# Optimization experiments

Hardware: AMD Instinct MI355X
Metric: run time of the kernel (lower is better)

The kernel has to match this reference:

```python
import jax, jax.numpy as jnp
import numpy as np

N = 8192
F_IN = 512
F_OUT = 512
DENSITY = 0.01


def setup_inputs() -> dict:
    key = jax.random.key(0)
    k_x, k_adj, k_w, k_b = jax.random.split(key, 4)
    input_features = jax.random.normal(k_x, (N, F_IN), dtype=jnp.float32)
    adj = (jax.random.uniform(k_adj, (N, N)) < DENSITY).astype(jnp.float32)
    idx = jnp.arange(N)
    adj = adj.at[idx, idx].set(1.0)
    # nn.Linear(in, out) params; W stored as [in, out] so hidden = x @ W + b
    W = jax.random.normal(k_w, (F_IN, F_OUT), dtype=jnp.float32) / np.sqrt(F_IN)
    b = jax.random.normal(k_b, (F_OUT,), dtype=jnp.float32) * 0.01
    return {"input_features": input_features, "adj": adj, "W": W, "b": b}


def reference(input_features, adj, W, b):
    # adj.to_dense().bool().float(): binarize any nonzero entry
    A = (adj != 0).astype(input_features.dtype)  # [N, N]
    hidden = input_features @ W + b              # [N, F_out]
    deg = jnp.sum(A, axis=0)                     # column sums, [N]
    return (A @ hidden) / deg[:, None]           # [N, F_out]
```

## Files before the change

### kernel.cpp

```cpp
#include <hip/hip_runtime.h>
#include <stdint.h>

#define N_NODES 8192
#define FEAT 512

__device__ __forceinline__ unsigned short f2bf(float f) {
  unsigned int u = __float_as_uint(f);
  u += 0x7fffu + ((u >> 16) & 1u);
  return (unsigned short)(u >> 16);
}
__device__ __forceinline__ float bflo(unsigned int u) { return __uint_as_float(u << 16); }
__device__ __forceinline__ float bfhi(unsigned int u) { return __uint_as_float(u & 0xffff0000u); }

typedef __attribute__((ext_vector_type(8))) short short8;
typedef __attribute__((ext_vector_type(4))) float floatx4;

__global__ __launch_bounds__(256) void prep_kernel(const float* __restrict__ W,
                                                   unsigned short* __restrict__ Wt,
                                                   unsigned int* __restrict__ deg) {
  int gid = blockIdx.x * 256 + threadIdx.x;
  int k = gid >> 9, n = gid & 511;
  Wt[n * 512 + k] = f2bf(W[gid]);
  if (gid < N_NODES) deg[gid] = 0u;
}

__global__ __launch_bounds__(512) void gemm_kernel(const float* __restrict__ x,
                                                   const unsigned short* __restrict__ Wt,
                                                   const float* __restrict__ bias,
                                                   unsigned short* __restrict__ hidden) {
  __shared__ __align__(16) unsigned short Ab[64][40];
  __shared__ __align__(16) unsigned short Bb[256][40];
  int t = threadIdx.x;
  int m0 = blockIdx.x * 64;
  int n0 = blockIdx.y * 256;
  int lane = t & 63, wave = t >> 6;
  int quad = lane >> 4, l15 = lane & 15;
  int wm = wave & 1, wn = wave >> 1;

  floatx4 acc[2][4];
#pragma unroll
  for (int i = 0; i < 2; ++i)
#pragma unroll
    for (int j = 0; j < 4; ++j) acc[i][j] = (floatx4)0.0f;

  int arow = t >> 3, ac = (t & 7) * 4;
  int brow = t >> 1, bc = (t & 1) * 16;
  const float* xa = x + (size_t)(m0 + arow) * 512 + ac;
  const unsigned short* wb = Wt + (size_t)(n0 + brow) * 512 + bc;

  for (int kt = 0; kt < 16; ++kt) {
    int k0 = kt * 32;
    __syncthreads();
    float4 av = *(const float4*)(xa + k0);
    uint2 aw;
    aw.x = (unsigned int)f2bf(av.x) | ((unsigned int)f2bf(av.y) << 16);
    aw.y = (unsigned int)f2bf(av.z) | ((unsigned int)f2bf(av.w) << 16);
    *(uint2*)&Ab[arow][ac] = aw;
    uint4 bv0 = *(const uint4*)(wb + k0);
    uint4 bv1 = *(const uint4*)(wb + k0 + 8);
    *(uint4*)&Bb[brow][bc] = bv0;
    *(uint4*)&Bb[brow][bc + 8] = bv1;
    __syncthreads();

    short8 af[2];
    short8 bfr[4];
#pragma unroll
    for (int im = 0; im < 2; ++im)
      af[im] = *(const short8*)&Ab[wm * 32 + im * 16 + l15][quad * 8];
#pragma unroll
    for (int jn = 0; jn < 4; ++jn)
      bfr[jn] = *(const short8*)&Bb[wn * 64 + jn * 16 + l15][quad * 8];
#pragma unroll
    for (int im = 0; im < 2; ++im)
#pragma unroll
      for (int jn = 0; jn < 4; ++jn)
        acc[im][jn] = __builtin_amdgcn_mfma_f32_16x16x32_bf16(af[im], bfr[jn], acc[im][jn], 0, 0, 0);
  }

#pragma unroll
  for (int jn = 0; jn < 4; ++jn) {
    int col = n0 + wn * 64 + jn * 16 + l15;
    float bb = bias[col];
#pragma unroll
    for (int im = 0; im < 2; ++im) {
#pragma unroll
      for (int rg = 0; rg < 4; ++rg) {
        int row = m0 + wm * 32 + im * 16 + quad * 4 + rg;
        hidden[(size_t)row * 512 + col] = f2bf(acc[im][jn][rg] + bb);
      }
    }
  }
}

#define PROC(val, e)                                                        \
  {                                                                         \
    bool nz = ((val) != 0.0f);                                              \
    if (nz) atomicAdd(&degl[base + 4 * lane + (e)], 1u);                    \
    unsigned long long m = __ballot(nz);                                    \
    while (m) {                                                             \
      int bit = __builtin_ctzll(m);                                         \
      m &= (m - 1);                                                         \
      int j = base + 4 * bit + (e);                                         \
      const uint2* hp = (const uint2*)(hidden + ((size_t)j << 9));          \
      uint2 h0 = hp[lane];                                                  \
      uint2 h1 = hp[64 + lane];                                             \
      acc[0] += bflo(h0.x); acc[1] += bfhi(h0.x);                           \
      acc[2] += bflo(h0.y); acc[3] += bfhi(h0.y);                           \
      acc[4] += bflo(h1.x); acc[5] += bfhi(h1.x);                           \
      acc[6] += bflo(h1.y); acc[7] += bfhi(h1.y);                           \
    }                                                                       \
  }

__global__ __launch_bounds__(256) void gather_kernel(const float* __restrict__ adj,
                                                     const unsigned short* __restrict__ hidden,
                                                     float* __restrict__ out,
                                                     unsigned int* __restrict__ deg) {
  __shared__ unsigned int degl[N_NODES];
  int tid = threadIdx.x;
#pragma unroll
  for (int i = 0; i < 32; ++i) degl[i * 256 + tid] = 0u;
  __syncthreads();

  int lane = tid & 63, wave = tid >> 6;
  int rbase = blockIdx.x * 8 + wave * 2;
  for (int rr = 0; rr < 2; ++rr) {
    int r = rbase + rr;
    const float4* __restrict__ arow = (const float4*)(adj + ((size_t)r << 13));
    float acc[8] = {0.f, 0.f, 0.f, 0.f, 0.f, 0.f, 0.f, 0.f};
    float4 cur = arow[lane];
    for (int ch = 0; ch < 32; ++ch) {
      float4 nxt = make_float4(0.f, 0.f, 0.f, 0.f);
      if (ch < 31) nxt = arow[(ch + 1) * 64 + lane];
      int base = ch * 256;
      PROC(cur.x, 0)
      PROC(cur.y, 1)
      PROC(cur.z, 2)
      PROC(cur.w, 3)
      cur = nxt;
    }
    float4* orow = (float4*)(out + ((size_t)r << 9));
    orow[lane] = make_float4(acc[0], acc[1], acc[2], acc[3]);
    orow[64 + lane] = make_float4(acc[4], acc[5], acc[6], acc[7]);
  }
  __syncthreads();
#pragma unroll
  for (int i = 0; i < 32; ++i) {
    unsigned int c = degl[i * 256 + tid];
    if (c) atomicAdd(&deg[i * 256 + tid], c);
  }
}

__global__ __launch_bounds__(256) void norm_kernel(float* __restrict__ out,
                                                   const unsigned int* __restrict__ deg) {
  int lane = threadIdx.x & 63, wave = threadIdx.x >> 6;
  int r = blockIdx.x * 4 + wave;
  float s = 1.0f / (float)deg[r];
  float4* p = (float4*)(out + ((size_t)r << 9));
  float4 v0 = p[lane], v1 = p[64 + lane];
  v0.x *= s; v0.y *= s; v0.z *= s; v0.w *= s;
  v1.x *= s; v1.y *= s; v1.z *= s; v1.w *= s;
  p[lane] = v0;
  p[64 + lane] = v1;
}

extern "C" void kernel_launch(void* const* d_in, const int* in_sizes, int n_in,
                              void* d_out, int out_size, void* d_ws, size_t ws_size,
                              hipStream_t stream) {
  const float* x   = (const float*)d_in[0];
  const float* adj = (const float*)d_in[1];
  const float* W   = (const float*)d_in[2];
  const float* b   = (const float*)d_in[3];
  float* out = (float*)d_out;

  char* ws = (char*)d_ws;
  unsigned short* hidden = (unsigned short*)ws;
  unsigned short* Wt     = (unsigned short*)(ws + (size_t)N_NODES * FEAT * 2);
  unsigned int*   deg    = (unsigned int*)(ws + (size_t)N_NODES * FEAT * 2 + (size_t)FEAT * FEAT * 2);

  prep_kernel<<<1024, 256, 0, stream>>>(W, Wt, deg);
  gemm_kernel<<<dim3(128, 2), 512, 0, stream>>>(x, Wt, b, hidden);
  gather_kernel<<<1024, 256, 0, stream>>>(adj, hidden, out, deg);
  norm_kernel<<<2048, 256, 0, stream>>>(out, deg);
}
```

Baseline: 463.2 us.

## Compact nonzero adjacency indices into per-wave LDS queue and batch gathers

Instead of gathering hidden rows serially per ballot bit, each wave compacts nonzero column indices into a shared-memory queue via ballot/popcount prefix. The queue is then drained with eight independent row loads in flight at a time, increasing memory-level parallelism for the gather. This adds LDS traffic and per-wave queue space, and the drain is issued between scanning chunks rather than inline with the scan.

```diff
diff --git a/kernel.cpp b/kernel.cpp
--- a/kernel.cpp
+++ b/kernel.cpp
@@ -3,6 +3,7 @@
 
 #define N_NODES 8192
 #define FEAT 512
+#define QCAP 1024
 
 __device__ __forceinline__ unsigned short f2bf(float f) {
   unsigned int u = __float_as_uint(f);
@@ -92,56 +93,87 @@
   }
 }
 
-#define PROC(val, e)                                                        \
-  {                                                                         \
-    bool nz = ((val) != 0.0f);                                              \
-    if (nz) atomicAdd(&degl[base + 4 * lane + (e)], 1u);                    \
-    unsigned long long m = __ballot(nz);                                    \
-    while (m) {                                                             \
-      int bit = __builtin_ctzll(m);                                         \
-      m &= (m - 1);                                                         \
-      int j = base + 4 * bit + (e);                                         \
-      const uint2* hp = (const uint2*)(hidden + ((size_t)j << 9));          \
-      uint2 h0 = hp[lane];                                                  \
-      uint2 h1 = hp[64 + lane];                                             \
-      acc[0] += bflo(h0.x); acc[1] += bfhi(h0.x);                           \
-      acc[2] += bflo(h0.y); acc[3] += bfhi(h0.y);                           \
-      acc[4] += bflo(h1.x); acc[5] += bfhi(h1.x);                           \
-      acc[6] += bflo(h1.y); acc[7] += bfhi(h1.y);                           \
-    }                                                                       \
-  }
-
 __global__ __launch_bounds__(256) void gather_kernel(const float* __restrict__ adj,
                                                      const unsigned short* __restrict__ hidden,
                                                      float* __restrict__ out,
                                                      unsigned int* __restrict__ deg) {
   __shared__ unsigned int degl[N_NODES];
+  __shared__ unsigned short q[4][QCAP];
   int tid = threadIdx.x;
 #pragma unroll
   for (int i = 0; i < 32; ++i) degl[i * 256 + tid] = 0u;
   __syncthreads();
 
   int lane = tid & 63, wave = tid >> 6;
+  unsigned short* wq = q[wave];
+  unsigned long long lanemask = (1ull << lane) - 1ull;
   int rbase = blockIdx.x * 8 + wave * 2;
+
   for (int rr = 0; rr < 2; ++rr) {
     int r = rbase + rr;
     const float4* __restrict__ arow = (const float4*)(adj + ((size_t)r << 13));
     float acc[8] = {0.f, 0.f, 0.f, 0.f, 0.f, 0.f, 0.f, 0.f};
+    int qcnt = 0;
+
+    auto drain = [&](int cnt) {
+      int i = 0;
+      for (; i + 8 <= cnt; i += 8) {
+        int jj[8];
+#pragma unroll
+        for (int d = 0; d < 8; ++d) jj[d] = wq[i + d];
+        uint2 h0[8], h1[8];
+#pragma unroll
+        for (int d = 0; d < 8; ++d) {
+          const uint2* hp = (const uint2*)(hidden + ((size_t)jj[d] << 9));
+          h0[d] = hp[lane];
+          h1[d] = hp[64 + lane];
+        }
+#pragma unroll
+        for (int d = 0; d < 8; ++d) {
+          acc[0] += bflo(h0[d].x); acc[1] += bfhi(h0[d].x);
+          acc[2] += bflo(h0[d].y); acc[3] += bfhi(h0[d].y);
+          acc[4] += bflo(h1[d].x); acc[5] += bfhi(h1[d].x);
+          acc[6] += bflo(h1[d].y); acc[7] += bfhi(h1[d].y);
+        }
+      }
+      for (; i < cnt; ++i) {
+        int j = wq[i];
+        const uint2* hp = (const uint2*)(hidden + ((size_t)j << 9));
+        uint2 h0 = hp[lane], h1 = hp[64 + lane];
+        acc[0] += bflo(h0.x); acc[1] += bfhi(h0.x);
+        acc[2] += bflo(h0.y); acc[3] += bfhi(h0.y);
+        acc[4] += bflo(h1.x); acc[5] += bfhi(h1.x);
+        acc[6] += bflo(h1.y); acc[7] += bfhi(h1.y);
+      }
+    };
+
     float4 cur = arow[lane];
     for (int ch = 0; ch < 32; ++ch) {
       float4 nxt = make_float4(0.f, 0.f, 0.f, 0.f);
       if (ch < 31) nxt = arow[(ch + 1) * 64 + lane];
-      int base = ch * 256;
-      PROC(cur.x, 0)
-      PROC(cur.y, 1)
-      PROC(cur.z, 2)
-      PROC(cur.w, 3)
+      if (qcnt > QCAP - 256) { drain(qcnt); qcnt = 0; }
+      int cbase = ch * 256 + 4 * lane;
+#pragma unroll
+      for (int e = 0; e < 4; ++e) {
+        float val = (e == 0) ? cur.x : (e == 1) ? cur.y : (e == 2) ? cur.z : cur.w;
+        bool nz = (val != 0.0f);
+        unsigned long long m = __ballot(nz);
+        if (nz) {
+          atomicAdd(&degl[cbase + e], 1u);
+          wq[qcnt + __popcll(m & lanemask)] = (unsigned short)(cbase + e);
+        }
+        qcnt += __popcll(m);
+      }
       cur = nxt;
     }
+
+    drain(qcnt);
+
     float4* orow = (float4*)(out + ((size_t)r << 9));
     orow[lane] = make_float4(acc[0], acc[1], acc[2], acc[3]);
     orow[64 + lane] = make_float4(acc[4], acc[5], acc[6], acc[7]);
   }
+
   __syncthreads();
 #pragma unroll
   for (int i = 0; i < 32; ++i) {
```

After: 448.0 us. -3.3%, faster.
